# Performance work log

Hardware: AMD Instinct MI355X
Metric: run time of the kernel (lower is better)

Reference implementation:

```python
import jax, jax.numpy as jnp
import numpy as np

D_IN = 1024
D_OUT = 1024
NUM_HEADS = 16
D_HEAD = D_OUT // NUM_HEADS


def setup_inputs() -> dict:
    key = jax.random.key(0)
    ks = jax.random.split(key, 6)
    s = 0.02
    return {
        "x": jax.random.normal(ks[0], (2, 2048, D_IN), dtype=jnp.float32),
        "W_q": jax.random.normal(ks[1], (D_IN, D_OUT), dtype=jnp.float32) * s,
        "W_k": jax.random.normal(ks[2], (D_IN, D_OUT), dtype=jnp.float32) * s,
        "W_v": jax.random.normal(ks[3], (D_IN, D_OUT), dtype=jnp.float32) * s,
        "W_o": jax.random.normal(ks[4], (D_OUT, D_OUT), dtype=jnp.float32) * s,
        "b_o": jax.random.normal(ks[5], (D_OUT,), dtype=jnp.float32) * s,
    }


def reference(x, W_q, W_k, W_v, W_o, b_o):
    B, T, _ = x.shape
    # qkv projections (no bias), split heads -> [B, H, T, d_head]
    def split_heads(t):
        return t.reshape(B, T, NUM_HEADS, D_HEAD).transpose(0, 2, 1, 3)
    q = split_heads(x @ W_q)
    k = split_heads(x @ W_k)
    v = split_heads(x @ W_v)
    # full causal scores [B, H, T, T]
    scores = jnp.einsum("bhqd,bhkd->bhqk", q, k)
    causal = jnp.triu(jnp.ones((T, T), dtype=bool), k=1)
    scores = jnp.where(causal, -jnp.inf, scores)
    attn = jax.nn.softmax(scores / np.sqrt(D_HEAD).astype(np.float32), axis=-1)
    # dropout rate is 0.0 -> identity
    ctx = jnp.einsum("bhqk,bhkd->bhqd", attn, v)
    ctx = ctx.transpose(0, 2, 1, 3).reshape(B, T, D_OUT)
    return ctx @ W_o + b_o
```

## Files before the change

### kernel.cpp

```cpp
#include <hip/hip_runtime.h>
#include <hip/hip_bf16.h>
#include <cstdint>

#define SEQ_T 2048
#define DMODEL 1024
#define NHEAD 16
#define DHEAD 64

typedef __attribute__((ext_vector_type(8))) __bf16 bf16x8;
typedef __attribute__((ext_vector_type(4))) float floatx4;

static __device__ __forceinline__ uint16_t f2bf(float f) {
    union { float f; uint32_t u; } v; v.f = f;
    uint32_t r = v.u + 0x7FFFu + ((v.u >> 16) & 1u);
    return (uint16_t)(r >> 16);
}

__global__ void mha_cvt_x(const float* __restrict__ x, uint16_t* __restrict__ xb) {
    int i = (blockIdx.x * blockDim.x + threadIdx.x) * 4;
    float4 f = *(const float4*)(x + i);
    union { uint16_t u[4]; uint64_t v; } o;
    o.u[0] = f2bf(f.x); o.u[1] = f2bf(f.y); o.u[2] = f2bf(f.z); o.u[3] = f2bf(f.w);
    *(uint64_t*)(xb + i) = o.v;
}

__global__ void mha_cvt_wt(const float* __restrict__ W0, const float* __restrict__ W1,
                           const float* __restrict__ W2, const float* __restrict__ W3,
                           uint16_t* __restrict__ T0, uint16_t* __restrict__ T1,
                           uint16_t* __restrict__ T2, uint16_t* __restrict__ T3) {
    const float* W; uint16_t* Tt;
    switch (blockIdx.z) {
        case 0: W = W0; Tt = T0; break;
        case 1: W = W1; Tt = T1; break;
        case 2: W = W2; Tt = T2; break;
        default: W = W3; Tt = T3; break;
    }
    __shared__ float tile[64][65];
    const int c  = threadIdx.x & 63;
    const int r0 = threadIdx.x >> 6;
    const int R0 = blockIdx.y * 64, C0 = blockIdx.x * 64;
#pragma unroll
    for (int rr = 0; rr < 16; ++rr) {
        int r = r0 + rr * 4;
        tile[r][c] = W[(size_t)(R0 + r) * DMODEL + C0 + c];
    }
    __syncthreads();
#pragma unroll
    for (int rr = 0; rr < 16; ++rr) {
        int r = r0 + rr * 4;
        Tt[(size_t)(C0 + r) * DMODEL + R0 + c] = f2bf(tile[c][r]);
    }
}

template<int MODE>
__device__ __forceinline__ void gemm64x128_body(
    const uint16_t* __restrict__ A, const uint16_t* __restrict__ Bt,
    uint16_t* __restrict__ outB) {
    const int K = DMODEL, N = DMODEL;
    __shared__ alignas(16) char smem[(MODE == 1) ? 18432 : 12288];
    uint16_t* As = (uint16_t*)smem;
    uint16_t* Bs = (uint16_t*)(smem + 4096);
    const int tid  = threadIdx.x;
    const int wave = tid >> 6;
    const int lane = tid & 63;
    const int m0 = blockIdx.y * 64;
    const int n0 = blockIdx.x * 128;
    const int lr   = lane & 15;
    const int quad = lane >> 4;

    floatx4 acc[4][2];
#pragma unroll
    for (int i = 0; i < 4; ++i)
#pragma unroll
        for (int j = 0; j < 2; ++j) acc[i][j] = (floatx4)0.0f;

    for (int k0 = 0; k0 < K; k0 += 32) {
#pragma unroll
        for (int it = 0; it < 3; ++it) {
            int c = it * 256 + wave * 64 + lane;
            if (it == 0) {
                int r = c >> 2, s = (c & 3) ^ ((r >> 1) & 3);
                const uint16_t* g = A + (size_t)(m0 + r) * K + k0 + s * 8;
                uint16_t* l = As + (size_t)c * 8;
                __builtin_amdgcn_global_load_lds((const __attribute__((address_space(1))) void*)g,
                                                 (__attribute__((address_space(3))) void*)l, 16, 0, 0);
            } else {
                int j = c - 256;
                int r = j >> 2, s = (j & 3) ^ ((r >> 1) & 3);
                const uint16_t* g = Bt + (size_t)(n0 + r) * K + k0 + s * 8;
                uint16_t* l = Bs + (size_t)j * 8;
                __builtin_amdgcn_global_load_lds((const __attribute__((address_space(1))) void*)g,
                                                 (__attribute__((address_space(3))) void*)l, 16, 0, 0);
            }
        }
        __syncthreads();
        bf16x8 af[4], bfr[2];
#pragma unroll
        for (int mi = 0; mi < 4; ++mi) {
            int row = mi * 16 + lr;
            af[mi] = *(const bf16x8*)&As[row * 32 + ((quad ^ ((row >> 1) & 3)) << 3)];
        }
#pragma unroll
        for (int ni = 0; ni < 2; ++ni) {
            int row = wave * 32 + ni * 16 + lr;
            bfr[ni] = *(const bf16x8*)&Bs[row * 32 + ((quad ^ ((row >> 1) & 3)) << 3)];
        }
#pragma unroll
        for (int mi = 0; mi < 4; ++mi)
#pragma unroll
            for (int ni = 0; ni < 2; ++ni)
                acc[mi][ni] = __builtin_amdgcn_mfma_f32_16x16x32_bf16(af[mi], bfr[ni], acc[mi][ni], 0, 0, 0);
        __syncthreads();
    }
    if constexpr (MODE == 1) {
        uint16_t* Ct = (uint16_t*)smem;
        const int bb = m0 >> 11, t0 = m0 & 2047;
#pragma unroll
        for (int mi = 0; mi < 4; ++mi)
#pragma unroll
            for (int ni = 0; ni < 2; ++ni) {
                int cl = wave * 32 + ni * 16 + lr;
                int tl = mi * 16 + quad * 4;
                int tls = tl ^ ((cl & 3) << 4);
                union { uint16_t u[4]; uint64_t v8; } pk;
#pragma unroll
                for (int r = 0; r < 4; ++r) pk.u[r] = f2bf(acc[mi][ni][r]);
                *(uint64_t*)&Ct[cl * 72 + tls] = pk.v8;
            }
        __syncthreads();
#pragma unroll
        for (int k = 0; k < 4; ++k) {
            int c = k * 256 + tid;
            int cl = c >> 3, off = (c & 7) * 8;
            int offs = off ^ ((cl & 3) << 4);
            uint4 v = *(const uint4*)&Ct[cl * 72 + offs];
            *(uint4*)&outB[((size_t)(bb * 1024 + n0 + cl)) * 2048 + t0 + off] = v;
        }
    } else {
#pragma unroll
        for (int mi = 0; mi < 4; ++mi)
#pragma unroll
            for (int ni = 0; ni < 2; ++ni) {
                int col = n0 + wave * 32 + ni * 16 + lr;
#pragma unroll
                for (int r = 0; r < 4; ++r) {
                    int row = m0 + mi * 16 + quad * 4 + r;
                    outB[(size_t)row * N + col] = f2bf(acc[mi][ni][r]);
                }
            }
    }
}

__global__ __launch_bounds__(256) void mha_gemm_qkv(
    const uint16_t* __restrict__ A,
    const uint16_t* __restrict__ Wq, const uint16_t* __restrict__ Wk, const uint16_t* __restrict__ Wv,
    uint16_t* __restrict__ Q, uint16_t* __restrict__ K, uint16_t* __restrict__ Vt) {
    switch (blockIdx.z) {
        case 0:  gemm64x128_body<0>(A, Wq, Q);  break;
        case 1:  gemm64x128_body<0>(A, Wk, K);  break;
        default: gemm64x128_body<1>(A, Wv, Vt); break;
    }
}

__global__ __launch_bounds__(256) void mha_gemm_out(
    const uint16_t* __restrict__ A, const uint16_t* __restrict__ Wot,
    float* __restrict__ out, const float* __restrict__ bias) {
    const int K = DMODEL, N = DMODEL;
    __shared__ alignas(16) uint16_t As[64 * 32];
    __shared__ alignas(16) uint16_t Bs[64 * 32];
    const int tid  = threadIdx.x;
    const int wave = tid >> 6;
    const int lane = tid & 63;
    const int m0 = blockIdx.y * 64;
    const int n0 = blockIdx.x * 64;
    const int lr   = lane & 15;
    const int quad = lane >> 4;

    floatx4 acc[4];
#pragma unroll
    for (int i = 0; i < 4; ++i) acc[i] = (floatx4)0.0f;

    for (int k0 = 0; k0 < K; k0 += 32) {
#pragma unroll
        for (int it = 0; it < 2; ++it) {
            int c = it * 256 + wave * 64 + lane;
            int j = c & 255;
            int r = j >> 2, s = (j & 3) ^ ((r >> 1) & 3);
            const uint16_t* g = (it == 0) ? (A   + (size_t)(m0 + r) * K + k0 + s * 8)
                                          : (Wot + (size_t)(n0 + r) * K + k0 + s * 8);
            uint16_t* l = ((it == 0) ? As : Bs) + (size_t)j * 8;
            __builtin_amdgcn_global_load_lds((const __attribute__((address_space(1))) void*)g,
                                             (__attribute__((address_space(3))) void*)l, 16, 0, 0);
        }
        __syncthreads();
        bf16x8 af[4], bfr;
#pragma unroll
        for (int mi = 0; mi < 4; ++mi) {
            int row = mi * 16 + lr;
            af[mi] = *(const bf16x8*)&As[row * 32 + ((quad ^ ((row >> 1) & 3)) << 3)];
        }
        {
            int row = wave * 16 + lr;
            bfr = *(const bf16x8*)&Bs[row * 32 + ((quad ^ ((row >> 1) & 3)) << 3)];
        }
#pragma unroll
        for (int mi = 0; mi < 4; ++mi)
            acc[mi] = __builtin_amdgcn_mfma_f32_16x16x32_bf16(af[mi], bfr, acc[mi], 0, 0, 0);
        __syncthreads();
    }
    int col = n0 + wave * 16 + lr;
    float bv = bias[col];
#pragma unroll
    for (int mi = 0; mi < 4; ++mi)
#pragma unroll
        for (int r = 0; r < 4; ++r) {
            int row = m0 + mi * 16 + quad * 4 + r;
            out[(size_t)row * N + col] = acc[mi][r] + bv;
        }
}

__global__ __launch_bounds__(256) void mha_attn_mfma(
    const uint16_t* __restrict__ Q, const uint16_t* __restrict__ K,
    const uint16_t* __restrict__ Vt, uint16_t* __restrict__ ctx) {
    __shared__ alignas(16) uint16_t Ks[2][64 * 64];
    __shared__ alignas(16) uint16_t Vs[2][64 * 64];
    __shared__ alignas(16) uint16_t Pb[64 * 72];

    const int tid  = threadIdx.x;
    const int wave = tid >> 6;
    const int lane = tid & 63;
    const int lr   = lane & 15;
    const int quad = lane >> 4;
    const int h  = blockIdx.x;
    const int p  = blockIdx.y;
    const int b  = blockIdx.z;
    const int jH = 31 - p, jL = p;
    const int TH = jH + 1;
    const int TL = jL + 1;
    const int Ttot = TH + TL;

    const uint16_t* kbase[2];
    const uint16_t* vbase[2];
#pragma unroll
    for (int i = 0; i < 2; ++i) {
        int c = i * 256 + tid;
        int row = c >> 3, cs = c & 7;
        int csk = cs ^ (row & 7);
        kbase[i] = K  + ((size_t)(b * SEQ_T) + row) * DMODEL + h * DHEAD + csk * 8;
        vbase[i] = Vt + ((size_t)(b * 1024 + h * DHEAD + row)) * 2048 + csk * 8;
    }

    int wrow = jH * 64 + wave * 16;
    bf16x8 qf0, qf1;
    {
        const size_t qb = ((size_t)(b * SEQ_T) + wrow + lr) * DMODEL + h * DHEAD;
        qf0 = *(const bf16x8*)(Q + qb + quad * 8);
        qf1 = *(const bf16x8*)(Q + qb + 32 + quad * 8);
    }
    floatx4 o[4];
#pragma unroll
    for (int nt = 0; nt < 4; ++nt) o[nt] = (floatx4)0.0f;
    float l[4] = {0.f, 0.f, 0.f, 0.f};

    auto stage = [&](int kv0, int buf) {
#pragma unroll
        for (int i = 0; i < 2; ++i) {
            const uint16_t* gk = kbase[i] + (size_t)kv0 * DMODEL;
            const uint16_t* gv = vbase[i] + kv0;
            uint16_t* lk = &Ks[buf][(i * 256 + wave * 64) * 8];
            uint16_t* lv = &Vs[buf][(i * 256 + wave * 64) * 8];
            __builtin_amdgcn_global_load_lds((const __attribute__((address_space(1))) void*)gk,
                                             (__attribute__((address_space(3))) void*)lk, 16, 0, 0);
            __builtin_amdgcn_global_load_lds((const __attribute__((address_space(1))) void*)gv,
                                             (__attribute__((address_space(3))) void*)lv, 16, 0, 0);
        }
    };
    auto epilogue = [&]() {
#pragma unroll
        for (int r = 0; r < 4; ++r) {
            float v = l[r];
            v += __shfl_xor(v, 1, 64);
            v += __shfl_xor(v, 2, 64);
            v += __shfl_xor(v, 4, 64);
            v += __shfl_xor(v, 8, 64);
            l[r] = 1.f / v;
        }
#pragma unroll
        for (int nt = 0; nt < 4; ++nt)
#pragma unroll
            for (int r = 0; r < 4; ++r) {
                size_t addr = ((size_t)(b * SEQ_T) + wrow + quad * 4 + r) * DMODEL + h * DHEAD + nt * 16 + lr;
                ctx[addr] = f2bf(o[nt][r] * l[r]);
            }
    };

    stage(0, 0);
    __syncthreads();
    int cur = 0;

    for (int t = 0; t < Ttot; ++t) {
        if (t + 1 < Ttot) {
            int nkv0 = ((t + 1 < TH) ? (t + 1) : (t + 1 - TH)) * 64;
            stage(nkv0, cur ^ 1);
        }
        const int kv0 = ((t < TH) ? t : (t - TH)) * 64;

        floatx4 s[4];
#pragma unroll
        for (int nt = 0; nt < 4; ++nt) {
            s[nt] = (floatx4)0.0f;
            int krow = nt * 16 + lr;
#pragma unroll
            for (int ks = 0; ks < 2; ++ks) {
                bf16x8 kf = *(const bf16x8*)&Ks[cur][krow * 64 + (((ks * 4 + quad) ^ (lr & 7)) * 8)];
                s[nt] = __builtin_amdgcn_mfma_f32_16x16x32_bf16(ks ? qf1 : qf0, kf, s[nt], 0, 0, 0);
            }
        }
        if (kv0 + 63 > wrow) {
#pragma unroll
            for (int nt = 0; nt < 4; ++nt) {
                int kcol = kv0 + nt * 16 + lr;
#pragma unroll
                for (int r = 0; r < 4; ++r) {
                    int qrow = wrow + quad * 4 + r;
                    if (kcol > qrow) s[nt][r] = -3e38f;
                }
            }
        }
#pragma unroll
        for (int nt = 0; nt < 4; ++nt)
#pragma unroll
            for (int r = 0; r < 4; ++r) {
                float pe = __expf(s[nt][r] * 0.125f);
                uint32_t pu = __float_as_uint(pe);
                l[r] += __uint_as_float(pu & 0xffff0000u);
                Pb[(wave * 16 + quad * 4 + r) * 72 + nt * 16 + lr] = (uint16_t)(pu >> 16);
            }
#pragma unroll
        for (int ks = 0; ks < 2; ++ks) {
            bf16x8 pfr = *(const bf16x8*)&Pb[(wave * 16 + lr) * 72 + ks * 32 + quad * 8];
#pragma unroll
            for (int nt = 0; nt < 4; ++nt) {
                int vrow = nt * 16 + lr;
                bf16x8 vf = *(const bf16x8*)&Vs[cur][vrow * 64 + (((ks * 4 + quad) ^ (lr & 7)) * 8)];
                o[nt] = __builtin_amdgcn_mfma_f32_16x16x32_bf16(pfr, vf, o[nt], 0, 0, 0);
            }
        }
        if (t == TH - 1) {
            epilogue();
            wrow = jL * 64 + wave * 16;
            const size_t qb = ((size_t)(b * SEQ_T) + wrow + lr) * DMODEL + h * DHEAD;
            qf0 = *(const bf16x8*)(Q + qb + quad * 8);
            qf1 = *(const bf16x8*)(Q + qb + 32 + quad * 8);
#pragma unroll
            for (int nt = 0; nt < 4; ++nt) o[nt] = (floatx4)0.0f;
#pragma unroll
            for (int r = 0; r < 4; ++r) l[r] = 0.f;
        }
        __syncthreads();
        cur ^= 1;
    }
    epilogue();
}

extern "C" void kernel_launch(void* const* d_in, const int* in_sizes, int n_in,
                              void* d_out, int out_size, void* d_ws, size_t ws_size,
                              hipStream_t stream) {
    const float* x  = (const float*)d_in[0];
    const float* Wq = (const float*)d_in[1];
    const float* Wk = (const float*)d_in[2];
    const float* Wv = (const float*)d_in[3];
    const float* Wo = (const float*)d_in[4];
    const float* bo = (const float*)d_in[5];
    float* out = (float*)d_out;

    char* ws = (char*)d_ws;
    const size_t SZ_X = (size_t)4096 * DMODEL * 2;
    const size_t SZ_W = (size_t)DMODEL * DMODEL * 2;
    size_t off = 0;
    uint16_t* xb  = (uint16_t*)(ws + off); off += SZ_X;
    uint16_t* wqt = (uint16_t*)(ws + off); off += SZ_W;
    uint16_t* wkt = (uint16_t*)(ws + off); off += SZ_W;
    uint16_t* wvt = (uint16_t*)(ws + off); off += SZ_W;
    uint16_t* wot = (uint16_t*)(ws + off); off += SZ_W;
    uint16_t* Qb  = (uint16_t*)(ws + off); off += SZ_X;
    uint16_t* Kb  = (uint16_t*)(ws + off); off += SZ_X;
    uint16_t* Vtb = (uint16_t*)(ws + off); off += SZ_X;
    uint16_t* Cb  = (uint16_t*)(ws + off); off += SZ_X;
    (void)ws_size; (void)in_sizes; (void)n_in; (void)out_size;

    mha_cvt_x<<<4096, 256, 0, stream>>>(x, xb);
    mha_cvt_wt<<<dim3(16, 16, 4), 256, 0, stream>>>(Wq, Wk, Wv, Wo, wqt, wkt, wvt, wot);
    mha_gemm_qkv<<<dim3(8, 64, 3), 256, 0, stream>>>(xb, wqt, wkt, wvt, Qb, Kb, Vtb);
    mha_attn_mfma<<<dim3(NHEAD, 16, 2), 256, 0, stream>>>(Qb, Kb, Vtb, Cb);
    mha_gemm_out<<<dim3(16, 64), 256, 0, stream>>>(Cb, wot, out, bo);
}
```

Before: 198.6 us.

## Fuse conversion kernels, share A tile across QKV, widen output GEMM tile

```diff
diff --git a/kernel.cpp b/kernel.cpp
--- a/kernel.cpp
+++ b/kernel.cpp
@@ -16,18 +16,23 @@
     return (uint16_t)(r >> 16);
 }
 
-__global__ void mha_cvt_x(const float* __restrict__ x, uint16_t* __restrict__ xb) {
-    int i = (blockIdx.x * blockDim.x + threadIdx.x) * 4;
-    float4 f = *(const float4*)(x + i);
-    union { uint16_t u[4]; uint64_t v; } o;
-    o.u[0] = f2bf(f.x); o.u[1] = f2bf(f.y); o.u[2] = f2bf(f.z); o.u[3] = f2bf(f.w);
-    *(uint64_t*)(xb + i) = o.v;
-}
-
-__global__ void mha_cvt_wt(const float* __restrict__ W0, const float* __restrict__ W1,
-                           const float* __restrict__ W2, const float* __restrict__ W3,
-                           uint16_t* __restrict__ T0, uint16_t* __restrict__ T1,
-                           uint16_t* __restrict__ T2, uint16_t* __restrict__ T3) {
+__global__ void mha_cvt(const float* __restrict__ x, uint16_t* __restrict__ xb,
+                        const float* __restrict__ W0, const float* __restrict__ W1,
+                        const float* __restrict__ W2, const float* __restrict__ W3,
+                        uint16_t* __restrict__ T0, uint16_t* __restrict__ T1,
+                        uint16_t* __restrict__ T2, uint16_t* __restrict__ T3) {
+    if (blockIdx.z == 4) {
+        int base = (blockIdx.y * 16 + blockIdx.x) * 256 + threadIdx.x;
+#pragma unroll
+        for (int i = 0; i < 16; ++i) {
+            int idx = base + i * 65536;
+            float4 f = ((const float4*)x)[idx];
+            union { uint16_t u[4]; uint64_t v; } o;
+            o.u[0] = f2bf(f.x); o.u[1] = f2bf(f.y); o.u[2] = f2bf(f.z); o.u[3] = f2bf(f.w);
+            ((uint64_t*)xb)[idx] = o.v;
+        }
+        return;
+    }
     const float* W; uint16_t* Tt;
     switch (blockIdx.z) {
         case 0: W = W0; Tt = T0; break;
@@ -52,14 +57,16 @@
     }
 }
 
-template<int MODE>
-__device__ __forceinline__ void gemm64x128_body(
-    const uint16_t* __restrict__ A, const uint16_t* __restrict__ Bt,
-    uint16_t* __restrict__ outB) {
-    const int K = DMODEL, N = DMODEL;
-    __shared__ alignas(16) char smem[(MODE == 1) ? 18432 : 12288];
+__global__ __launch_bounds__(256) void mha_gemm_qkv(
+    const uint16_t* __restrict__ A,
+    const uint16_t* __restrict__ Wq, const uint16_t* __restrict__ Wk, const uint16_t* __restrict__ Wv,
+    uint16_t* __restrict__ Q, uint16_t* __restrict__ K, uint16_t* __restrict__ Vt) {
+    const int Kd = DMODEL;
+    __shared__ alignas(16) char smem[4096 + 3 * 8192];
     uint16_t* As = (uint16_t*)smem;
-    uint16_t* Bs = (uint16_t*)(smem + 4096);
+    uint16_t* Bs[3] = { (uint16_t*)(smem + 4096), (uint16_t*)(smem + 12288),
+                        (uint16_t*)(smem + 20480) };
+    const uint16_t* Wt[3] = { Wq, Wk, Wv };
     const int tid  = threadIdx.x;
     const int wave = tid >> 6;
     const int lane = tid & 63;
@@ -68,75 +75,58 @@
     const int lr   = lane & 15;
     const int quad = lane >> 4;
 
-    floatx4 acc[4][2];
-#pragma unroll
-    for (int i = 0; i < 4; ++i)
-#pragma unroll
-        for (int j = 0; j < 2; ++j) acc[i][j] = (floatx4)0.0f;
-
-    for (int k0 = 0; k0 < K; k0 += 32) {
-#pragma unroll
-        for (int it = 0; it < 3; ++it) {
-            int c = it * 256 + wave * 64 + lane;
-            if (it == 0) {
+    floatx4 acc[3][4][2];
+#pragma unroll
+    for (int w = 0; w < 3; ++w)
+#pragma unroll
+        for (int i = 0; i < 4; ++i)
+#pragma unroll
+            for (int j = 0; j < 2; ++j) acc[w][i][j] = (floatx4)0.0f;
+
+    for (int k0 = 0; k0 < Kd; k0 += 32) {
+        {
+            int c = tid;
+            int r = c >> 2, s = (c & 3) ^ ((r >> 1) & 3);
+            const uint16_t* g = A + (size_t)(m0 + r) * Kd + k0 + s * 8;
+            __builtin_amdgcn_global_load_lds((const __attribute__((address_space(1))) void*)g,
+                                             (__attribute__((address_space(3))) void*)(As + (size_t)c * 8), 16, 0, 0);
+        }
+#pragma unroll
+        for (int w = 0; w < 3; ++w)
+#pragma unroll
+            for (int it = 0; it < 2; ++it) {
+                int c = it * 256 + tid;
                 int r = c >> 2, s = (c & 3) ^ ((r >> 1) & 3);
-                const uint16_t* g = A + (size_t)(m0 + r) * K + k0 + s * 8;
-                uint16_t* l = As + (size_t)c * 8;
+                const uint16_t* g = Wt[w] + (size_t)(n0 + r) * Kd + k0 + s * 8;
                 __builtin_amdgcn_global_load_lds((const __attribute__((address_space(1))) void*)g,
-                                                 (__attribute__((address_space(3))) void*)l, 16, 0, 0);
-            } else {
-                int j = c - 256;
-                int r = j >> 2, s = (j & 3) ^ ((r >> 1) & 3);
-                const uint16_t* g = Bt + (size_t)(n0 + r) * K + k0 + s * 8;
-                uint16_t* l = Bs + (size_t)j * 8;
-                __builtin_amdgcn_global_load_lds((const __attribute__((address_space(1))) void*)g,
-                                                 (__attribute__((address_space(3))) void*)l, 16, 0, 0);
-            }
-        }
+                                                 (__attribute__((address_space(3))) void*)(Bs[w] + (size_t)c * 8), 16, 0, 0);
+            }
         __syncthreads();
-        bf16x8 af[4], bfr[2];
+        bf16x8 af[4];
 #pragma unroll
         for (int mi = 0; mi < 4; ++mi) {
             int row = mi * 16 + lr;
             af[mi] = *(const bf16x8*)&As[row * 32 + ((quad ^ ((row >> 1) & 3)) << 3)];
         }
 #pragma unroll
-        for (int ni = 0; ni < 2; ++ni) {
-            int row = wave * 32 + ni * 16 + lr;
-            bfr[ni] = *(const bf16x8*)&Bs[row * 32 + ((quad ^ ((row >> 1) & 3)) << 3)];
-        }
-#pragma unroll
-        for (int mi = 0; mi < 4; ++mi)
-#pragma unroll
-            for (int ni = 0; ni < 2; ++ni)
-                acc[mi][ni] = __builtin_amdgcn_mfma_f32_16x16x32_bf16(af[mi], bfr[ni], acc[mi][ni], 0, 0, 0);
+        for (int w = 0; w < 3; ++w) {
+            bf16x8 bfr[2];
+#pragma unroll
+            for (int ni = 0; ni < 2; ++ni) {
+                int row = wave * 32 + ni * 16 + lr;
+                bfr[ni] = *(const bf16x8*)&Bs[w][row * 32 + ((quad ^ ((row >> 1) & 3)) << 3)];
+            }
+#pragma unroll
+            for (int mi = 0; mi < 4; ++mi)
+#pragma unroll
+                for (int ni = 0; ni < 2; ++ni)
+                    acc[w][mi][ni] = __builtin_amdgcn_mfma_f32_16x16x32_bf16(af[mi], bfr[ni], acc[w][mi][ni], 0, 0, 0);
+        }
         __syncthreads();
     }
-    if constexpr (MODE == 1) {
-        uint16_t* Ct = (uint16_t*)smem;
-        const int bb = m0 >> 11, t0 = m0 & 2047;
-#pragma unroll
-        for (int mi = 0; mi < 4; ++mi)
-#pragma unroll
-            for (int ni = 0; ni < 2; ++ni) {
-                int cl = wave * 32 + ni * 16 + lr;
-                int tl = mi * 16 + quad * 4;
-                int tls = tl ^ ((cl & 3) << 4);
-                union { uint16_t u[4]; uint64_t v8; } pk;
-#pragma unroll
-                for (int r = 0; r < 4; ++r) pk.u[r] = f2bf(acc[mi][ni][r]);
-                *(uint64_t*)&Ct[cl * 72 + tls] = pk.v8;
-            }
-        __syncthreads();
-#pragma unroll
-        for (int k = 0; k < 4; ++k) {
-            int c = k * 256 + tid;
-            int cl = c >> 3, off = (c & 7) * 8;
-            int offs = off ^ ((cl & 3) << 4);
-            uint4 v = *(const uint4*)&Ct[cl * 72 + offs];
-            *(uint4*)&outB[((size_t)(bb * 1024 + n0 + cl)) * 2048 + t0 + off] = v;
-        }
-    } else {
+#pragma unroll
+    for (int w = 0; w < 2; ++w) {
+        uint16_t* outp = (w == 0) ? Q : K;
 #pragma unroll
         for (int mi = 0; mi < 4; ++mi)
 #pragma unroll
@@ -145,20 +135,32 @@
 #pragma unroll
                 for (int r = 0; r < 4; ++r) {
                     int row = m0 + mi * 16 + quad * 4 + r;
-                    outB[(size_t)row * N + col] = f2bf(acc[mi][ni][r]);
+                    outp[(size_t)row * DMODEL + col] = f2bf(acc[w][mi][ni][r]);
                 }
             }
     }
-}
-
-__global__ __launch_bounds__(256) void mha_gemm_qkv(
-    const uint16_t* __restrict__ A,
-    const uint16_t* __restrict__ Wq, const uint16_t* __restrict__ Wk, const uint16_t* __restrict__ Wv,
-    uint16_t* __restrict__ Q, uint16_t* __restrict__ K, uint16_t* __restrict__ Vt) {
-    switch (blockIdx.z) {
-        case 0:  gemm64x128_body<0>(A, Wq, Q);  break;
-        case 1:  gemm64x128_body<0>(A, Wk, K);  break;
-        default: gemm64x128_body<1>(A, Wv, Vt); break;
+    uint16_t* Ct = (uint16_t*)smem;
+    const int bb = m0 >> 11, t0 = m0 & 2047;
+#pragma unroll
+    for (int mi = 0; mi < 4; ++mi)
+#pragma unroll
+        for (int ni = 0; ni < 2; ++ni) {
+            int cl = wave * 32 + ni * 16 + lr;
+            int tl = mi * 16 + quad * 4;
+            int tls = tl ^ ((cl & 3) << 4);
+            union { uint16_t u[4]; uint64_t v8; } pk;
+#pragma unroll
+            for (int r = 0; r < 4; ++r) pk.u[r] = f2bf(acc[2][mi][ni][r]);
+            *(uint64_t*)&Ct[cl * 72 + tls] = pk.v8;
+        }
+    __syncthreads();
+#pragma unroll
+    for (int k = 0; k < 4; ++k) {
+        int c = k * 256 + tid;
+        int cl = c >> 3, off = (c & 7) * 8;
+        int offs = off ^ ((cl & 3) << 4);
+        uint4 v = *(const uint4*)&Ct[cl * 72 + offs];
+        *(uint4*)&Vt[((size_t)(bb * 1024 + n0 + cl)) * 2048 + t0 + off] = v;
     }
 }
 
@@ -167,55 +169,67 @@
     float* __restrict__ out, const float* __restrict__ bias) {
     const int K = DMODEL, N = DMODEL;
     __shared__ alignas(16) uint16_t As[64 * 32];
-    __shared__ alignas(16) uint16_t Bs[64 * 32];
+    __shared__ alignas(16) uint16_t Bs[128 * 32];
     const int tid  = threadIdx.x;
     const int wave = tid >> 6;
     const int lane = tid & 63;
     const int m0 = blockIdx.y * 64;
-    const int n0 = blockIdx.x * 64;
+    const int n0 = blockIdx.x * 128;
     const int lr   = lane & 15;
     const int quad = lane >> 4;
 
-    floatx4 acc[4];
-#pragma unroll
-    for (int i = 0; i < 4; ++i) acc[i] = (floatx4)0.0f;
+    floatx4 acc[4][2];
+#pragma unroll
+    for (int i = 0; i < 4; ++i)
+#pragma unroll
+        for (int j = 0; j < 2; ++j) acc[i][j] = (floatx4)0.0f;
 
     for (int k0 = 0; k0 < K; k0 += 32) {
+        {
+            int c = tid;
+            int r = c >> 2, s = (c & 3) ^ ((r >> 1) & 3);
+            const uint16_t* g = A + (size_t)(m0 + r) * K + k0 + s * 8;
+            __builtin_amdgcn_global_load_lds((const __attribute__((address_space(1))) void*)g,
+                                             (__attribute__((address_space(3))) void*)(As + (size_t)c * 8), 16, 0, 0);
+        }
 #pragma unroll
         for (int it = 0; it < 2; ++it) {
-            int c = it * 256 + wave * 64 + lane;
-            int j = c & 255;
-            int r = j >> 2, s = (j & 3) ^ ((r >> 1) & 3);
-            const uint16_t* g = (it == 0) ? (A   + (size_t)(m0 + r) * K + k0 + s * 8)
-                                          : (Wot + (size_t)(n0 + r) * K + k0 + s * 8);
-            uint16_t* l = ((it == 0) ? As : Bs) + (size_t)j * 8;
+            int c = it * 256 + tid;
+            int r = c >> 2, s = (c & 3) ^ ((r >> 1) & 3);
+            const uint16_t* g = Wot + (size_t)(n0 + r) * K + k0 + s * 8;
             __builtin_amdgcn_global_load_lds((const __attribute__((address_space(1))) void*)g,
-                                             (__attribute__((address_space(3))) void*)l, 16, 0, 0);
+                                             (__attribute__((address_space(3))) void*)(Bs + (size_t)c * 8), 16, 0, 0);
         }
         __syncthreads();
-        bf16x8 af[4], bfr;
+        bf16x8 af[4], bfr[2];
 #pragma unroll
         for (int mi = 0; mi < 4; ++mi) {
             int row = mi * 16 + lr;
             af[mi] = *(const bf16x8*)&As[row * 32 + ((quad ^ ((row >> 1) & 3)) << 3)];
         }
-        {
-            int row = wave * 16 + lr;
-            bfr = *(const bf16x8*)&Bs[row * 32 + ((quad ^ ((row >> 1) & 3)) << 3)];
+#pragma unroll
+        for (int ni = 0; ni < 2; ++ni) {
+            int row = wave * 32 + ni * 16 + lr;
+            bfr[ni] = *(const bf16x8*)&Bs[row * 32 + ((quad ^ ((row >> 1) & 3)) << 3)];
         }
 #pragma unroll
         for (int mi = 0; mi < 4; ++mi)
-            acc[mi] = __builtin_amdgcn_mfma_f32_16x16x32_bf16(af[mi], bfr, acc[mi], 0, 0, 0);
+#pragma unroll
+            for (int ni = 0; ni < 2; ++ni)
+                acc[mi][ni] = __builtin_amdgcn_mfma_f32_16x16x32_bf16(af[mi], bfr[ni], acc[mi][ni], 0, 0, 0);
         __syncthreads();
     }
-    int col = n0 + wave * 16 + lr;
-    float bv = bias[col];
 #pragma unroll
     for (int mi = 0; mi < 4; ++mi)
 #pragma unroll
-        for (int r = 0; r < 4; ++r) {
-            int row = m0 + mi * 16 + quad * 4 + r;
-            out[(size_t)row * N + col] = acc[mi][r] + bv;
+        for (int ni = 0; ni < 2; ++ni) {
+            int col = n0 + wave * 32 + ni * 16 + lr;
+            float bv = bias[col];
+#pragma unroll
+            for (int r = 0; r < 4; ++r) {
+                int row = m0 + mi * 16 + quad * 4 + r;
+                out[(size_t)row * N + col] = acc[mi][ni][r] + bv;
+            }
         }
 }
 
@@ -389,9 +403,8 @@
     uint16_t* Cb  = (uint16_t*)(ws + off); off += SZ_X;
     (void)ws_size; (void)in_sizes; (void)n_in; (void)out_size;
 
-    mha_cvt_x<<<4096, 256, 0, stream>>>(x, xb);
-    mha_cvt_wt<<<dim3(16, 16, 4), 256, 0, stream>>>(Wq, Wk, Wv, Wo, wqt, wkt, wvt, wot);
-    mha_gemm_qkv<<<dim3(8, 64, 3), 256, 0, stream>>>(xb, wqt, wkt, wvt, Qb, Kb, Vtb);
+    mha_cvt<<<dim3(16, 16, 5), 256, 0, stream>>>(x, xb, Wq, Wk, Wv, Wo, wqt, wkt, wvt, wot);
+    mha_gemm_qkv<<<dim3(8, 64), 256, 0, stream>>>(xb, wqt, wkt, wvt, Qb, Kb, Vtb);
     mha_attn_mfma<<<dim3(NHEAD, 16, 2), 256, 0, stream>>>(Qb, Kb, Vtb, Cb);
-    mha_gemm_out<<<dim3(16, 64), 256, 0, stream>>>(Cb, wot, out, bo);
-}
+    mha_gemm_out<<<dim3(8, 64), 256, 0, stream>>>(Cb, wot, out, bo);
+}
```

Measured after the change: 219.2 us. 10.4% more time.

## Deepen GEMM K-tile to 64, share body with output GEMM, merge conversion kernels

Applied to the files above, without the earlier changes.

```diff
diff --git a/kernel.cpp b/kernel.cpp
--- a/kernel.cpp
+++ b/kernel.cpp
@@ -16,18 +16,23 @@
     return (uint16_t)(r >> 16);
 }
 
-__global__ void mha_cvt_x(const float* __restrict__ x, uint16_t* __restrict__ xb) {
-    int i = (blockIdx.x * blockDim.x + threadIdx.x) * 4;
-    float4 f = *(const float4*)(x + i);
-    union { uint16_t u[4]; uint64_t v; } o;
-    o.u[0] = f2bf(f.x); o.u[1] = f2bf(f.y); o.u[2] = f2bf(f.z); o.u[3] = f2bf(f.w);
-    *(uint64_t*)(xb + i) = o.v;
-}
-
-__global__ void mha_cvt_wt(const float* __restrict__ W0, const float* __restrict__ W1,
-                           const float* __restrict__ W2, const float* __restrict__ W3,
-                           uint16_t* __restrict__ T0, uint16_t* __restrict__ T1,
-                           uint16_t* __restrict__ T2, uint16_t* __restrict__ T3) {
+__global__ void mha_cvt(const float* __restrict__ x, uint16_t* __restrict__ xb,
+                        const float* __restrict__ W0, const float* __restrict__ W1,
+                        const float* __restrict__ W2, const float* __restrict__ W3,
+                        uint16_t* __restrict__ T0, uint16_t* __restrict__ T1,
+                        uint16_t* __restrict__ T2, uint16_t* __restrict__ T3) {
+    if (blockIdx.z == 4) {
+        int base = (blockIdx.y * 16 + blockIdx.x) * 256 + threadIdx.x;
+#pragma unroll
+        for (int i = 0; i < 16; ++i) {
+            int idx = base + i * 65536;
+            float4 f = ((const float4*)x)[idx];
+            union { uint16_t u[4]; uint64_t v; } o;
+            o.u[0] = f2bf(f.x); o.u[1] = f2bf(f.y); o.u[2] = f2bf(f.z); o.u[3] = f2bf(f.w);
+            ((uint64_t*)xb)[idx] = o.v;
+        }
+        return;
+    }
     const float* W; uint16_t* Tt;
     switch (blockIdx.z) {
         case 0: W = W0; Tt = T0; break;
@@ -53,13 +58,14 @@
 }
 
 template<int MODE>
-__device__ __forceinline__ void gemm64x128_body(
+__device__ __forceinline__ void gemm_bk64_body(
     const uint16_t* __restrict__ A, const uint16_t* __restrict__ Bt,
-    uint16_t* __restrict__ outB) {
+    uint16_t* __restrict__ outB, float* __restrict__ outF,
+    const float* __restrict__ bias) {
     const int K = DMODEL, N = DMODEL;
-    __shared__ alignas(16) char smem[(MODE == 1) ? 18432 : 12288];
+    __shared__ alignas(16) char smem[24576];
     uint16_t* As = (uint16_t*)smem;
-    uint16_t* Bs = (uint16_t*)(smem + 4096);
+    uint16_t* Bs = (uint16_t*)(smem + 8192);
     const int tid  = threadIdx.x;
     const int wave = tid >> 6;
     const int lane = tid & 63;
@@ -74,42 +80,43 @@
 #pragma unroll
         for (int j = 0; j < 2; ++j) acc[i][j] = (floatx4)0.0f;
 
-    for (int k0 = 0; k0 < K; k0 += 32) {
-#pragma unroll
-        for (int it = 0; it < 3; ++it) {
-            int c = it * 256 + wave * 64 + lane;
-            if (it == 0) {
-                int r = c >> 2, s = (c & 3) ^ ((r >> 1) & 3);
-                const uint16_t* g = A + (size_t)(m0 + r) * K + k0 + s * 8;
-                uint16_t* l = As + (size_t)c * 8;
-                __builtin_amdgcn_global_load_lds((const __attribute__((address_space(1))) void*)g,
-                                                 (__attribute__((address_space(3))) void*)l, 16, 0, 0);
-            } else {
-                int j = c - 256;
-                int r = j >> 2, s = (j & 3) ^ ((r >> 1) & 3);
-                const uint16_t* g = Bt + (size_t)(n0 + r) * K + k0 + s * 8;
-                uint16_t* l = Bs + (size_t)j * 8;
-                __builtin_amdgcn_global_load_lds((const __attribute__((address_space(1))) void*)g,
-                                                 (__attribute__((address_space(3))) void*)l, 16, 0, 0);
-            }
+    for (int k0 = 0; k0 < K; k0 += 64) {
+#pragma unroll
+        for (int i = 0; i < 2; ++i) {
+            int c = i * 256 + tid;
+            int r = c >> 3, s = (c & 7) ^ (r & 7);
+            const uint16_t* g = A + (size_t)(m0 + r) * K + k0 + s * 8;
+            __builtin_amdgcn_global_load_lds((const __attribute__((address_space(1))) void*)g,
+                                             (__attribute__((address_space(3))) void*)(As + (size_t)c * 8), 16, 0, 0);
+        }
+#pragma unroll
+        for (int i = 0; i < 4; ++i) {
+            int c = i * 256 + tid;
+            int r = c >> 3, s = (c & 7) ^ (r & 7);
+            const uint16_t* g = Bt + (size_t)(n0 + r) * K + k0 + s * 8;
+            __builtin_amdgcn_global_load_lds((const __attribute__((address_space(1))) void*)g,
+                                             (__attribute__((address_space(3))) void*)(Bs + (size_t)c * 8), 16, 0, 0);
         }
         __syncthreads();
-        bf16x8 af[4], bfr[2];
-#pragma unroll
-        for (int mi = 0; mi < 4; ++mi) {
-            int row = mi * 16 + lr;
-            af[mi] = *(const bf16x8*)&As[row * 32 + ((quad ^ ((row >> 1) & 3)) << 3)];
-        }
-#pragma unroll
-        for (int ni = 0; ni < 2; ++ni) {
-            int row = wave * 32 + ni * 16 + lr;
-            bfr[ni] = *(const bf16x8*)&Bs[row * 32 + ((quad ^ ((row >> 1) & 3)) << 3)];
-        }
-#pragma unroll
-        for (int mi = 0; mi < 4; ++mi)
-#pragma unroll
-            for (int ni = 0; ni < 2; ++ni)
-                acc[mi][ni] = __builtin_amdgcn_mfma_f32_16x16x32_bf16(af[mi], bfr[ni], acc[mi][ni], 0, 0, 0);
+#pragma unroll
+        for (int ks = 0; ks < 2; ++ks) {
+            bf16x8 af[4], bfr[2];
+#pragma unroll
+            for (int mi = 0; mi < 4; ++mi) {
+                int row = mi * 16 + lr;
+                af[mi] = *(const bf16x8*)&As[row * 64 + (((ks * 4 + quad) ^ (row & 7)) << 3)];
+            }
+#pragma unroll
+            for (int ni = 0; ni < 2; ++ni) {
+                int row = wave * 32 + ni * 16 + lr;
+                bfr[ni] = *(const bf16x8*)&Bs[row * 64 + (((ks * 4 + quad) ^ (row & 7)) << 3)];
+            }
+#pragma unroll
+            for (int mi = 0; mi < 4; ++mi)
+#pragma unroll
+                for (int ni = 0; ni < 2; ++ni)
+                    acc[mi][ni] = __builtin_amdgcn_mfma_f32_16x16x32_bf16(af[mi], bfr[ni], acc[mi][ni], 0, 0, 0);
+        }
         __syncthreads();
     }
     if constexpr (MODE == 1) {
@@ -136,6 +143,19 @@
             uint4 v = *(const uint4*)&Ct[cl * 72 + offs];
             *(uint4*)&outB[((size_t)(bb * 1024 + n0 + cl)) * 2048 + t0 + off] = v;
         }
+    } else if constexpr (MODE == 2) {
+#pragma unroll
+        for (int mi = 0; mi < 4; ++mi)
+#pragma unroll
+            for (int ni = 0; ni < 2; ++ni) {
+                int col = n0 + wave * 32 + ni * 16 + lr;
+                float bv = bias[col];
+#pragma unroll
+                for (int r = 0; r < 4; ++r) {
+                    int row = m0 + mi * 16 + quad * 4 + r;
+                    outF[(size_t)row * N + col] = acc[mi][ni][r] + bv;
+                }
+            }
     } else {
 #pragma unroll
         for (int mi = 0; mi < 4; ++mi)
@@ -156,67 +176,16 @@
     const uint16_t* __restrict__ Wq, const uint16_t* __restrict__ Wk, const uint16_t* __restrict__ Wv,
     uint16_t* __restrict__ Q, uint16_t* __restrict__ K, uint16_t* __restrict__ Vt) {
     switch (blockIdx.z) {
-        case 0:  gemm64x128_body<0>(A, Wq, Q);  break;
-        case 1:  gemm64x128_body<0>(A, Wk, K);  break;
-        default: gemm64x128_body<1>(A, Wv, Vt); break;
+        case 0:  gemm_bk64_body<0>(A, Wq, Q,  nullptr, nullptr); break;
+        case 1:  gemm_bk64_body<0>(A, Wk, K,  nullptr, nullptr); break;
+        default: gemm_bk64_body<1>(A, Wv, Vt, nullptr, nullptr); break;
     }
 }
 
 __global__ __launch_bounds__(256) void mha_gemm_out(
     const uint16_t* __restrict__ A, const uint16_t* __restrict__ Wot,
     float* __restrict__ out, const float* __restrict__ bias) {
-    const int K = DMODEL, N = DMODEL;
-    __shared__ alignas(16) uint16_t As[64 * 32];
-    __shared__ alignas(16) uint16_t Bs[64 * 32];
-    const int tid  = threadIdx.x;
-    const int wave = tid >> 6;
-    const int lane = tid & 63;
-    const int m0 = blockIdx.y * 64;
-    const int n0 = blockIdx.x * 64;
-    const int lr   = lane & 15;
-    const int quad = lane >> 4;
-
-    floatx4 acc[4];
-#pragma unroll
-    for (int i = 0; i < 4; ++i) acc[i] = (floatx4)0.0f;
-
-    for (int k0 = 0; k0 < K; k0 += 32) {
-#pragma unroll
-        for (int it = 0; it < 2; ++it) {
-            int c = it * 256 + wave * 64 + lane;
-            int j = c & 255;
-            int r = j >> 2, s = (j & 3) ^ ((r >> 1) & 3);
-            const uint16_t* g = (it == 0) ? (A   + (size_t)(m0 + r) * K + k0 + s * 8)
-                                          : (Wot + (size_t)(n0 + r) * K + k0 + s * 8);
-            uint16_t* l = ((it == 0) ? As : Bs) + (size_t)j * 8;
-            __builtin_amdgcn_global_load_lds((const __attribute__((address_space(1))) void*)g,
-                                             (__attribute__((address_space(3))) void*)l, 16, 0, 0);
-        }
-        __syncthreads();
-        bf16x8 af[4], bfr;
-#pragma unroll
-        for (int mi = 0; mi < 4; ++mi) {
-            int row = mi * 16 + lr;
-            af[mi] = *(const bf16x8*)&As[row * 32 + ((quad ^ ((row >> 1) & 3)) << 3)];
-        }
-        {
-            int row = wave * 16 + lr;
-            bfr = *(const bf16x8*)&Bs[row * 32 + ((quad ^ ((row >> 1) & 3)) << 3)];
-        }
-#pragma unroll
-        for (int mi = 0; mi < 4; ++mi)
-            acc[mi] = __builtin_amdgcn_mfma_f32_16x16x32_bf16(af[mi], bfr, acc[mi], 0, 0, 0);
-        __syncthreads();
-    }
-    int col = n0 + wave * 16 + lr;
-    float bv = bias[col];
-#pragma unroll
-    for (int mi = 0; mi < 4; ++mi)
-#pragma unroll
-        for (int r = 0; r < 4; ++r) {
-            int row = m0 + mi * 16 + quad * 4 + r;
-            out[(size_t)row * N + col] = acc[mi][r] + bv;
-        }
+    gemm_bk64_body<2>(A, Wot, nullptr, out, bias);
 }
 
 __global__ __launch_bounds__(256) void mha_attn_mfma(
@@ -389,9 +358,8 @@
     uint16_t* Cb  = (uint16_t*)(ws + off); off += SZ_X;
     (void)ws_size; (void)in_sizes; (void)n_in; (void)out_size;
 
-    mha_cvt_x<<<4096, 256, 0, stream>>>(x, xb);
-    mha_cvt_wt<<<dim3(16, 16, 4), 256, 0, stream>>>(Wq, Wk, Wv, Wo, wqt, wkt, wvt, wot);
+    mha_cvt<<<dim3(16, 16, 5), 256, 0, stream>>>(x, xb, Wq, Wk, Wv, Wo, wqt, wkt, wvt, wot);
     mha_gemm_qkv<<<dim3(8, 64, 3), 256, 0, stream>>>(xb, wqt, wkt, wvt, Qb, Kb, Vtb);
     mha_attn_mfma<<<dim3(NHEAD, 16, 2), 256, 0, stream>>>(Qb, Kb, Vtb, Cb);
-    mha_gemm_out<<<dim3(16, 64), 256, 0, stream>>>(Cb, wot, out, bo);
-}
+    mha_gemm_out<<<dim3(8, 64), 256, 0, stream>>>(Cb, wot, out, bo);
+}
```

New measurement: 181.8 us. 8.4% less time.
